# Performance work log

Measured on AMD Instinct MI355X. Metric: run time of the kernel, lower is better.

The kernel has to match this reference:

```python
import jax, jax.numpy as jnp
import numpy as np

N = 96   # collocation points per axis
H = 64   # MLP hidden width (features[:-1])
R = 32   # CP rank (r * out_dim with out_dim=1)


def setup_inputs() -> dict:
    key = jax.random.key(0)
    ks = jax.random.split(key, 7)

    def glorot(k, shape, fan_in, fan_out):
        s = np.sqrt(2.0 / (fan_in + fan_out)).astype(np.float32)
        return jax.random.normal(k, shape, jnp.float32) * s

    return {
        "t": jax.random.uniform(ks[0], (N, 1), jnp.float32),
        "x": jax.random.uniform(ks[1], (N, 1), jnp.float32),
        "y": jax.random.uniform(ks[2], (N, 1), jnp.float32),
        "z": jax.random.uniform(ks[3], (N, 1), jnp.float32),
        "W1": glorot(ks[4], (4, 1, H), 1, H),
        "b1": jnp.zeros((4, H), jnp.float32),
        "W2": glorot(ks[5], (4, H, H), H, H),
        "b2": jnp.zeros((4, H), jnp.float32),
        "W3": glorot(ks[6], (4, H, R), H, R),
        "b3": jnp.zeros((4, R), jnp.float32),
    }


def reference(t, x, y, z, W1, b1, W2, b2, W3, b3):
    coords = (t, x, y, z)
    outs = []
    for i in range(4):  # fixed small loop over the 4 axes (distinct params)
        h = jnp.tanh(coords[i] @ W1[i] + b1[i])   # [N, H]
        h = jnp.tanh(h @ W2[i] + b2[i])           # [N, H]
        o = h @ W3[i] + b3[i]                     # [N, R]
        outs.append(o.T)                          # [R, N]
    ft, fx, fy, fz = outs
    tx = jnp.einsum('ft,fx->ftx', ft, fx)         # [R, Nt, Nx]
    txy = jnp.einsum('ftx,fy->ftxy', tx, fy)      # [R, Nt, Nx, Ny]
    pred = jnp.einsum('ftxy,fz->txyz', txy, fz)   # [Nt, Nx, Ny, Nz]
    return pred
```

## Files before the change

### kernel.cpp

```cpp
#include <hip/hip_runtime.h>

#define NPTS 96
#define HID  64
#define RANK 32

typedef float f2 __attribute__((ext_vector_type(2)));

#define TRANS_OFF (4 * RANK * NPTS)

__global__ __launch_bounds__(64) void spinn_mlp(
    const float* __restrict__ t, const float* __restrict__ x,
    const float* __restrict__ y, const float* __restrict__ z,
    const float* __restrict__ W1, const float* __restrict__ b1,
    const float* __restrict__ W2, const float* __restrict__ b2,
    const float* __restrict__ W3, const float* __restrict__ b3,
    float* __restrict__ ws)
{
    const int n    = blockIdx.x;
    const int axis = blockIdx.y;
    const int j    = threadIdx.x;

    const float* coords[4] = { t, x, y, z };
    const float c = coords[axis][n];

    __shared__ float h1[HID];
    __shared__ float h2[HID];

    h1[j] = tanhf(fmaf(c, W1[axis * HID + j], b1[axis * HID + j]));
    __syncthreads();

    float a = b2[axis * HID + j];
    #pragma unroll
    for (int k = 0; k < HID; ++k)
        a = fmaf(h1[k], W2[(axis * HID + k) * HID + j], a);
    h2[j] = tanhf(a);
    __syncthreads();

    if (j < RANK) {
        float o = b3[axis * RANK + j];
        #pragma unroll
        for (int k = 0; k < HID; ++k)
            o = fmaf(h2[k], W3[(axis * HID + k) * RANK + j], o);
        ws[axis * RANK * NPTS + j * NPTS + n]        = o;
        ws[TRANS_OFF + (axis * NPTS + n) * RANK + j] = o;
    }
}

__global__ __launch_bounds__(192, 4) void spinn_outer(
    const float* __restrict__ ws, float* __restrict__ out)
{
    const int tt  = blockIdx.x;
    const int yb  = blockIdx.y;
    const int xh  = blockIdx.z;
    const int tid = threadIdx.x;
    const int zp  = tid % 48;
    const int yq  = tid / 48;
    const int yy  = yb * 4 + yq;
    const int z0  = zp * 2;

    const float* ftT = ws + TRANS_OFF + (0 * NPTS + tt) * RANK;
    const float* fyT = ws + TRANS_OFF + (2 * NPTS + yy) * RANK;
    const float* fzP = ws + 3 * RANK * NPTS;

    f2 q2[16][2];
    #pragma unroll
    for (int k = 0; k < 16; ++k) {
        const f2 ft2 = *(const f2*)(ftT + 2 * k);
        const f2 fy2 = *(const f2*)(fyT + 2 * k);
        const float g0 = ft2.x * fy2.x;
        const float g1 = ft2.y * fy2.y;
        const f2 za = *(const f2*)(fzP + (2 * k) * NPTS + z0);
        const f2 zb = *(const f2*)(fzP + (2 * k + 1) * NPTS + z0);
        q2[k][0] = f2{ g0 * za.x, g1 * zb.x };
        q2[k][1] = f2{ g0 * za.y, g1 * zb.y };
    }

    const int x0 = xh * 24;
    const float* fxT = ws + TRANS_OFF + (1 * NPTS) * RANK;
    float* outp = out + (size_t)tt * NPTS * NPTS * NPTS
                      + (size_t)x0 * NPTS * NPTS
                      + (size_t)yy * NPTS + z0;

    #pragma unroll 2
    for (int xs = 0; xs < 24; ++xs) {
        const f2* fp = (const f2*)(fxT + (size_t)(x0 + xs) * RANK);
        f2 a0 = { 0.f, 0.f }, a1 = { 0.f, 0.f };
        #pragma unroll
        for (int k = 0; k < 16; ++k) {
            const f2 p = fp[k];
            a0 = __builtin_elementwise_fma(p, q2[k][0], a0);
            a1 = __builtin_elementwise_fma(p, q2[k][1], a1);
        }
        const f2 r = { a0.x + a0.y, a1.x + a1.y };
        *(f2*)outp = r;
        outp += NPTS * NPTS;
    }
}

extern "C" void kernel_launch(void* const* d_in, const int* in_sizes, int n_in,
                              void* d_out, int out_size, void* d_ws, size_t ws_size,
                              hipStream_t stream)
{
    const float* t  = (const float*)d_in[0];
    const float* x  = (const float*)d_in[1];
    const float* y  = (const float*)d_in[2];
    const float* z  = (const float*)d_in[3];
    const float* W1 = (const float*)d_in[4];
    const float* b1 = (const float*)d_in[5];
    const float* W2 = (const float*)d_in[6];
    const float* b2 = (const float*)d_in[7];
    const float* W3 = (const float*)d_in[8];
    const float* b3 = (const float*)d_in[9];

    float* ws  = (float*)d_ws;
    float* out = (float*)d_out;

    spinn_mlp<<<dim3(NPTS, 4), 64, 0, stream>>>(t, x, y, z, W1, b1, W2, b2, W3, b3, ws);
    spinn_outer<<<dim3(NPTS, 24, 4), 192, 0, stream>>>(ws, out);
}
```

Baseline: 86.55 us.

## Restructure outer-product kernel to per-(t,x) blocks looping over y with contiguous slabs

Each block now handles one (t,x) pair and loops over y in chunks of 8 rows. It writes a contiguous 96x96 output slab and keeps ft*fx and fz factors in registers. The MLP now stores only the transposed factor layout, which drops the duplicate store. The aim is more contiguous stores and fewer factor reloads, at the cost of an extra multiply per rank term in the inner loop.

Result: slower. 278.3 us (+221.6%).

```diff
diff --git a/kernel.cpp b/kernel.cpp
--- a/kernel.cpp
+++ b/kernel.cpp
@@ -6,7 +6,7 @@
 
 typedef float f2 __attribute__((ext_vector_type(2)));
 
-#define TRANS_OFF (4 * RANK * NPTS)
+#define TR(axis, n) ((((axis) * NPTS) + (n)) * RANK)
 
 __global__ __launch_bounds__(64) void spinn_mlp(
     const float* __restrict__ t, const float* __restrict__ x,
@@ -41,59 +41,53 @@
         #pragma unroll
         for (int k = 0; k < HID; ++k)
             o = fmaf(h2[k], W3[(axis * HID + k) * RANK + j], o);
-        ws[axis * RANK * NPTS + j * NPTS + n]        = o;
-        ws[TRANS_OFF + (axis * NPTS + n) * RANK + j] = o;
+        ws[TR(axis, n) + j] = o;
     }
 }
 
-__global__ __launch_bounds__(192, 4) void spinn_outer(
+__global__ __launch_bounds__(384, 3) void spinn_recon(
     const float* __restrict__ ws, float* __restrict__ out)
 {
-    const int tt  = blockIdx.x;
-    const int yb  = blockIdx.y;
-    const int xh  = blockIdx.z;
+    const int xx  = blockIdx.x;
+    const int tt  = blockIdx.y;
     const int tid = threadIdx.x;
+    const int y8  = tid / 48;
     const int zp  = tid % 48;
-    const int yq  = tid / 48;
-    const int yy  = yb * 4 + yq;
     const int z0  = zp * 2;
 
-    const float* ftT = ws + TRANS_OFF + (0 * NPTS + tt) * RANK;
-    const float* fyT = ws + TRANS_OFF + (2 * NPTS + yy) * RANK;
-    const float* fzP = ws + 3 * RANK * NPTS;
+    const float* ftR = ws + TR(0, tt);
+    const float* fxR = ws + TR(1, xx);
+    const float* fzR0 = ws + TR(3, z0);
+    const float* fzR1 = ws + TR(3, z0 + 1);
+
+    f2 A2[16];
+    #pragma unroll
+    for (int k = 0; k < 16; ++k)
+        A2[k] = *(const f2*)(ftR + 2 * k) * *(const f2*)(fxR + 2 * k);
 
     f2 q2[16][2];
     #pragma unroll
     for (int k = 0; k < 16; ++k) {
-        const f2 ft2 = *(const f2*)(ftT + 2 * k);
-        const f2 fy2 = *(const f2*)(fyT + 2 * k);
-        const float g0 = ft2.x * fy2.x;
-        const float g1 = ft2.y * fy2.y;
-        const f2 za = *(const f2*)(fzP + (2 * k) * NPTS + z0);
-        const f2 zb = *(const f2*)(fzP + (2 * k + 1) * NPTS + z0);
-        q2[k][0] = f2{ g0 * za.x, g1 * zb.x };
-        q2[k][1] = f2{ g0 * za.y, g1 * zb.y };
+        q2[k][0] = *(const f2*)(fzR0 + 2 * k);
+        q2[k][1] = *(const f2*)(fzR1 + 2 * k);
     }
 
-    const int x0 = xh * 24;
-    const float* fxT = ws + TRANS_OFF + (1 * NPTS) * RANK;
-    float* outp = out + (size_t)tt * NPTS * NPTS * NPTS
-                      + (size_t)x0 * NPTS * NPTS
-                      + (size_t)yy * NPTS + z0;
+    float* outb = out + ((size_t)tt * NPTS + xx) * (NPTS * NPTS) + z0;
 
-    #pragma unroll 2
-    for (int xs = 0; xs < 24; ++xs) {
-        const f2* fp = (const f2*)(fxT + (size_t)(x0 + xs) * RANK);
+    #pragma unroll 1
+    for (int yb = 0; yb < 12; ++yb) {
+        const int yy = yb * 8 + y8;
+        const float* fyR = ws + TR(2, yy);
+
         f2 a0 = { 0.f, 0.f }, a1 = { 0.f, 0.f };
         #pragma unroll
         for (int k = 0; k < 16; ++k) {
-            const f2 p = fp[k];
-            a0 = __builtin_elementwise_fma(p, q2[k][0], a0);
-            a1 = __builtin_elementwise_fma(p, q2[k][1], a1);
+            const f2 g2 = A2[k] * *(const f2*)(fyR + 2 * k);
+            a0 = __builtin_elementwise_fma(g2, q2[k][0], a0);
+            a1 = __builtin_elementwise_fma(g2, q2[k][1], a1);
         }
         const f2 r = { a0.x + a0.y, a1.x + a1.y };
-        *(f2*)outp = r;
-        outp += NPTS * NPTS;
+        *(f2*)(outb + (size_t)yy * NPTS) = r;
     }
 }
 
@@ -116,5 +110,5 @@
     float* out = (float*)d_out;
 
     spinn_mlp<<<dim3(NPTS, 4), 64, 0, stream>>>(t, x, y, z, W1, b1, W2, b2, W3, b3, ws);
-    spinn_outer<<<dim3(NPTS, 24, 4), 192, 0, stream>>>(ws, out);
+    spinn_recon<<<dim3(NPTS, NPTS), 384, 0, stream>>>(ws, out);
 }
```
